# Kernel tuning notes

Hardware: AMD Instinct MI355X
Metric: run time of the kernel (lower is better)

The kernel has to match this reference:

```python
import jax, jax.numpy as jnp
import numpy as np

B, P, S, D, H, DFF, VOC = 16, 10, 128, 512, 8, 2048, 32000
SIGMA = 0.05
LN_EPS = 1e-6


def _ln(x, g, b):
    mu = jnp.mean(x, axis=-1, keepdims=True)
    var = jnp.var(x, axis=-1, keepdims=True)
    return g * (x - mu) / jnp.sqrt(var + LN_EPS) + b


def setup_inputs() -> dict:
    key = jax.random.key(0)
    ks = jax.random.split(key, 16)
    def wmat(k, shp):
        return (jax.random.normal(k, shp) * 0.02).astype(jnp.float32)
    return {
        "r": jax.random.normal(ks[0], (B, P, D), jnp.float32),
        "x": jax.random.randint(ks[1], (B,), 0, VOC),
        "K": jax.random.normal(ks[2], (B, P, S, D), jnp.float32),
        "V": jax.random.normal(ks[3], (B, P, S, D), jnp.float32),
        "w_state": jax.random.uniform(ks[4], (B, P, 1), jnp.float32),
        "I": jax.random.randint(ks[5], (B, P, S), 0, P),
        "t": 64,
        "Wq": wmat(ks[6], (D, D)), "bq": jnp.zeros((D,), jnp.float32),
        "Wk": wmat(ks[7], (D, D)), "bk": jnp.zeros((D,), jnp.float32),
        "Wv": wmat(ks[8], (D, D)), "bv": jnp.zeros((D,), jnp.float32),
        "Wo": wmat(ks[9], (D, D)), "bo": jnp.zeros((D,), jnp.float32),
        "W1": wmat(ks[10], (D, DFF)), "b1": jnp.zeros((DFF,), jnp.float32),
        "W2": wmat(ks[11], (DFF, D)), "b2": jnp.zeros((D,), jnp.float32),
        "g1": jnp.ones((D,), jnp.float32), "be1": jnp.zeros((D,), jnp.float32),
        "g3": jnp.ones((D,), jnp.float32), "be3": jnp.zeros((D,), jnp.float32),
        "Wout": wmat(ks[12], (D, VOC)), "bout": jnp.zeros((VOC,), jnp.float32),
    }


def reference(r, x, K, V, w_state, I, t, Wq, bq, Wk, bk, Wv, bv, Wo, bo,
              W1, b1, W2, b2, g1, be1, g3, be3, Wout, bout):
    k1, k2, k3, k4, k5 = jax.random.split(jax.random.key(42), 5)
    I = I.astype(jnp.int32)
    # particle resampling of attention state: gather along particle dim per timestep
    K = jnp.take_along_axis(K, I[..., None], axis=1)  # (B,P,S,D)
    V = jnp.take_along_axis(V, I[..., None], axis=1)
    rin = r[:, :, None, :]                            # (B,P,1,D)
    q = rin @ Wq + bq
    k = rin @ Wk + bk
    v = rin @ Wv + bv
    # SMC reparameterization noise on the projections
    q = q + SIGMA * jax.random.normal(k1, q.shape, q.dtype)
    k = k + SIGMA * jax.random.normal(k2, k.shape, k.dtype)
    v = v + SIGMA * jax.random.normal(k3, v.shape, v.dtype)
    # write current k, v into the attention state at position t
    K = jax.lax.dynamic_update_slice_in_dim(K, k, t, axis=2)
    V = jax.lax.dynamic_update_slice_in_dim(V, v, t, axis=2)
    dh = D // H
    qh = q.reshape(B, P, 1, H, dh).transpose(0, 1, 3, 2, 4)  # (B,P,H,1,dh)
    Kh = K.reshape(B, P, S, H, dh).transpose(0, 1, 3, 2, 4)  # (B,P,H,S,dh)
    Vh = V.reshape(B, P, S, H, dh).transpose(0, 1, 3, 2, 4)
    scores = jnp.einsum('bphqd,bphsd->bphqs', qh, Kh) / jnp.sqrt(jnp.asarray(dh, q.dtype))
    attn = jax.nn.softmax(scores, axis=-1)                   # (B,P,H,1,S)
    ctx = jnp.einsum('bphqs,bphsd->bphqd', attn, Vh)
    ctx = ctx.transpose(0, 1, 3, 2, 4).reshape(B, P, 1, D)
    z = ctx @ Wo + bo
    epsilon = SIGMA * jax.random.normal(k4, z.shape, z.dtype)  # stored stddev
    z = z + epsilon
    attn_weights = jnp.mean(attn, axis=2)                    # (B,P,1,S)
    out1 = _ln(z + rin, g1, be1)
    ffn = jax.nn.relu(out1 @ W1 + b1) @ W2 + b2
    out3 = _ln(ffn + out1, g3, be3)                          # (B,P,1,D)
    predictions = out3 @ Wout + bout                         # (B,P,1,VOC)
    # classification weight computation: softmax + gather at label x
    probs = jax.nn.softmax(predictions, axis=-1)
    w = jnp.take_along_axis(probs, x[:, None, None, None].astype(jnp.int32), axis=-1)[..., 0, 0]  # (B,P)
    w = jax.lax.stop_gradient(w)
    pred_sq = predictions[:, :, 0, :]                        # (B,P,VOC)
    average_prediction = jnp.sum(pred_sq * w[:, :, None], axis=1)[:, None, :]  # (B,1,VOC)
    argmax_w = jnp.argmax(w, axis=1)
    max_prediction = jnp.take_along_axis(pred_sq, argmax_w[:, None, None], axis=1)[:, 0, :]  # (B,VOC)
    # sample-and-keep-indices: categorical draw of P particle ancestors per batch
    i_t = jax.random.categorical(k5, w[:, None, :], axis=-1, shape=(B, P)).astype(jnp.int32)
    I_new = jax.lax.dynamic_update_slice_in_dim(I, i_t[:, :, None], t, axis=2)
    I_new = jax.lax.stop_gradient(I_new)
    # resample z with the freshly-sampled indices (I_new[:,:,t] == i_t)
    z = jnp.take_along_axis(z, i_t[:, :, None, None], axis=1)
    return out3, z, average_prediction, max_prediction, epsilon, attn_weights, K, V, w, I_new
```

## Files before the change

### kernel.cpp

```cpp
#include <hip/hip_runtime.h>
#include <cstdint>
#include <cstddef>

#define B_    16
#define P_    10
#define S_    128
#define D_    512
#define H_    8
#define DH_   64
#define DFF_  2048
#define VOC_  32000
#define NROW  160
#define SIGMA 0.05f
#define LN_EPS 1e-6f

struct U2 { uint32_t x, y; };

__host__ __device__ __forceinline__ U2 tf2x32(uint32_t k0, uint32_t k1,
                                              uint32_t x0, uint32_t x1) {
  uint32_t ks[3] = {k0, k1, k0 ^ k1 ^ 0x1BD11BDAu};
  x0 += ks[0]; x1 += ks[1];
  const int R0[4] = {13, 15, 26, 6};
  const int R1[4] = {17, 29, 16, 24};
#pragma unroll
  for (int i = 0; i < 5; ++i) {
    const int* r = (i & 1) ? R1 : R0;
#pragma unroll
    for (int j = 0; j < 4; ++j) {
      x0 += x1;
      x1 = (x1 << r[j]) | (x1 >> (32 - r[j]));
      x1 ^= x0;
    }
    x0 += ks[(i + 1) % 3];
    x1 += ks[(i + 2) % 3] + (uint32_t)(i + 1);
  }
  return {x0, x1};
}

__device__ __forceinline__ uint32_t jax_bits32(uint32_t k0, uint32_t k1, uint32_t j) {
  U2 o = tf2x32(k0, k1, 0u, j);
  return o.x ^ o.y;
}

__device__ __forceinline__ float erfinv32(float x) {
  float w = -log1pf(-x * x);
  float p;
  if (w < 5.0f) {
    w = w - 2.5f;
    p = 2.81022636e-08f;
    p = fmaf(p, w, 3.43273939e-07f);
    p = fmaf(p, w, -3.5233877e-06f);
    p = fmaf(p, w, -4.39150654e-06f);
    p = fmaf(p, w, 0.00021858087f);
    p = fmaf(p, w, -0.00125372503f);
    p = fmaf(p, w, -0.00417768164f);
    p = fmaf(p, w, 0.246640727f);
    p = fmaf(p, w, 1.50140941f);
  } else {
    w = sqrtf(w) - 3.0f;
    p = -0.000200214257f;
    p = fmaf(p, w, 0.000100950558f);
    p = fmaf(p, w, 0.00134934322f);
    p = fmaf(p, w, -0.00367342844f);
    p = fmaf(p, w, 0.00573950773f);
    p = fmaf(p, w, -0.0076224613f);
    p = fmaf(p, w, 0.00943887047f);
    p = fmaf(p, w, 1.00167406f);
    p = fmaf(p, w, 2.83297682f);
  }
  return p * x;
}

__device__ __forceinline__ float jax_normal(uint32_t k0, uint32_t k1, uint32_t j) {
  uint32_t b = jax_bits32(k0, k1, j);
  float u01 = __uint_as_float((b >> 9) | 0x3F800000u) - 1.0f;
  const float lo = -0.99999994f;
  float u = fmaxf(lo, fmaf(u01, 2.0f, lo));
  return 1.41421356f * erfinv32(u);
}

__device__ __forceinline__ float jax_gumbel(uint32_t k0, uint32_t k1, uint32_t j) {
  uint32_t b = jax_bits32(k0, k1, j);
  float u01 = __uint_as_float((b >> 9) | 0x3F800000u) - 1.0f;
  const float tiny = 1.17549435e-38f;
  float u = fmaxf(tiny, u01 + tiny);
  return -logf(-logf(u));
}


__global__ __launch_bounds__(256) void k_gather(const float* __restrict__ K,
                                                const float* __restrict__ V,
                                                const int* __restrict__ I,
                                                float* __restrict__ oK,
                                                float* __restrict__ oV) {
  size_t idx = (size_t)blockIdx.x * 256 + threadIdx.x;
  const size_t total = (size_t)NROW * S_ * (D_ / 4);
  if (idx >= total) return;
  int d4 = (int)(idx % (D_ / 4));
  size_t row = idx / (D_ / 4);
  int s = (int)(row % S_);
  int bp = (int)(row / S_);
  int b = bp / P_;
  int iv = I[row];
  size_t src = ((size_t)(b * P_ + iv) * S_ + s) * (D_ / 4) + d4;
  ((float4*)oK)[idx] = ((const float4*)K)[src];
  ((float4*)oV)[idx] = ((const float4*)V)[src];
}

__global__ __launch_bounds__(128) void k_qkvp(const float* __restrict__ r,
    const float* __restrict__ Wq, const float* __restrict__ bq,
    const float* __restrict__ Wk, const float* __restrict__ bk,
    const float* __restrict__ Wv, const float* __restrict__ bv,
    float* __restrict__ pq, float* __restrict__ pk, float* __restrict__ pv) {
  int c = blockIdx.x * 128 + threadIdx.x;
  int r0 = blockIdx.y * 4;
  int kc = blockIdx.z;
  int d0 = kc * 64;
  float aq[4], ak[4], av[4];
  float bbq = (kc == 0) ? bq[c] : 0.f;
  float bbk = (kc == 0) ? bk[c] : 0.f;
  float bbv = (kc == 0) ? bv[c] : 0.f;
#pragma unroll
  for (int rr = 0; rr < 4; ++rr) { aq[rr] = bbq; ak[rr] = bbk; av[rr] = bbv; }
  for (int d = d0; d < d0 + 64; d += 4) {
    float wq0 = Wq[(size_t)d * D_ + c],      wq1 = Wq[(size_t)(d+1) * D_ + c];
    float wq2 = Wq[(size_t)(d+2) * D_ + c],  wq3 = Wq[(size_t)(d+3) * D_ + c];
    float wk0 = Wk[(size_t)d * D_ + c],      wk1 = Wk[(size_t)(d+1) * D_ + c];
    float wk2 = Wk[(size_t)(d+2) * D_ + c],  wk3 = Wk[(size_t)(d+3) * D_ + c];
    float wv0 = Wv[(size_t)d * D_ + c],      wv1 = Wv[(size_t)(d+1) * D_ + c];
    float wv2 = Wv[(size_t)(d+2) * D_ + c],  wv3 = Wv[(size_t)(d+3) * D_ + c];
#pragma unroll
    for (int rr = 0; rr < 4; ++rr) {
      float4 a = *(const float4*)&r[(size_t)(r0 + rr) * D_ + d];
      aq[rr] = fmaf(a.w, wq3, fmaf(a.z, wq2, fmaf(a.y, wq1, fmaf(a.x, wq0, aq[rr]))));
      ak[rr] = fmaf(a.w, wk3, fmaf(a.z, wk2, fmaf(a.y, wk1, fmaf(a.x, wk0, ak[rr]))));
      av[rr] = fmaf(a.w, wv3, fmaf(a.z, wv2, fmaf(a.y, wv1, fmaf(a.x, wv0, av[rr]))));
    }
  }
#pragma unroll
  for (int rr = 0; rr < 4; ++rr) {
    size_t o = ((size_t)kc * NROW + r0 + rr) * D_ + c;
    pq[o] = aq[rr]; pk[o] = ak[rr]; pv[o] = av[rr];
  }
}

__global__ __launch_bounds__(256) void k_qkvr(const float* __restrict__ pq,
    const float* __restrict__ pk, const float* __restrict__ pv,
    const int* __restrict__ tptr, float* __restrict__ wsq,
    float* __restrict__ oK, float* __restrict__ oV,
    uint32_t k1a, uint32_t k1b, uint32_t k2a, uint32_t k2b,
    uint32_t k3a, uint32_t k3b) {
  int idx = blockIdx.x * 256 + threadIdx.x;
  if (idx >= NROW * D_) return;
  float q = pq[idx], k = pk[idx], v = pv[idx];
#pragma unroll
  for (int kc = 1; kc < 8; ++kc) {
    size_t o = (size_t)kc * (NROW * D_) + idx;
    q += pq[o]; k += pk[o]; v += pv[o];
  }
  int bp = idx / D_, c = idx % D_;
  int ts = min(max(*tptr, 0), S_ - 1);
  uint32_t j = (uint32_t)idx;
  wsq[idx] = q + SIGMA * jax_normal(k1a, k1b, j);
  oK[((size_t)bp * S_ + ts) * D_ + c] = k + SIGMA * jax_normal(k2a, k2b, j);
  oV[((size_t)bp * S_ + ts) * D_ + c] = v + SIGMA * jax_normal(k3a, k3b, j);
}

__global__ __launch_bounds__(128) void k_attn(const float* __restrict__ wsq,
    const float* __restrict__ oK, const float* __restrict__ oV,
    float* __restrict__ wsctx, float* __restrict__ wsattn) {
  __shared__ float s_q[DH_];
  __shared__ float s_attn[S_];
  __shared__ float red[S_];
  int bp = blockIdx.x >> 3, h = blockIdx.x & 7, tid = threadIdx.x;
  if (tid < DH_) s_q[tid] = wsq[bp * D_ + h * DH_ + tid];
  __syncthreads();
  const float4* krow = (const float4*)(oK + ((size_t)bp * S_ + tid) * D_ + h * DH_);
  const float4* q4 = (const float4*)s_q;
  float sc = 0.f;
#pragma unroll
  for (int d = 0; d < DH_ / 4; ++d) {
    float4 kv = krow[d], qv = q4[d];
    sc += qv.x * kv.x + qv.y * kv.y + qv.z * kv.z + qv.w * kv.w;
  }
  sc *= 0.125f;
  red[tid] = sc; __syncthreads();
  for (int s = 64; s > 0; s >>= 1) {
    if (tid < s) red[tid] = fmaxf(red[tid], red[tid + s]);
    __syncthreads();
  }
  float m = red[0]; __syncthreads();
  float e = expf(sc - m);
  red[tid] = e; __syncthreads();
  for (int s = 64; s > 0; s >>= 1) {
    if (tid < s) red[tid] += red[tid + s];
    __syncthreads();
  }
  float a = e / red[0];
  s_attn[tid] = a;
  wsattn[(size_t)blockIdx.x * S_ + tid] = a;
  __syncthreads();
  {
    int dd = tid & 63, sh = tid >> 6;
    const float* vb = oV + ((size_t)bp * S_ + sh * 64) * D_ + h * DH_ + dd;
    float acc = 0.f;
#pragma unroll 4
    for (int s = 0; s < 64; ++s) acc = fmaf(s_attn[sh * 64 + s], vb[(size_t)s * D_], acc);
    red[tid] = acc; __syncthreads();
    if (tid < DH_) wsctx[bp * D_ + h * DH_ + tid] = red[tid] + red[tid + 64];
  }
}

__global__ __launch_bounds__(256) void k_aw(const float* __restrict__ wsattn,
                                            float* __restrict__ oaw) {
  int idx = blockIdx.x * 256 + threadIdx.x;
  if (idx >= NROW * S_) return;
  int bp = idx / S_, s = idx % S_;
  float acc = 0.f;
#pragma unroll
  for (int h = 0; h < H_; ++h) acc += wsattn[(size_t)(bp * H_ + h) * S_ + s];
  oaw[idx] = acc * 0.125f;
}

__global__ __launch_bounds__(128) void k_zmatp(const float* __restrict__ wsctx,
    const float* __restrict__ Wo, const float* __restrict__ bo,
    float* __restrict__ pz) {
  int c = blockIdx.x * 128 + threadIdx.x;
  int r0 = blockIdx.y * 4;
  int kc = blockIdx.z;
  int d0 = kc * 64;
  float acc[4];
  float bb = (kc == 0) ? bo[c] : 0.f;
#pragma unroll
  for (int rr = 0; rr < 4; ++rr) acc[rr] = bb;
  for (int d = d0; d < d0 + 64; d += 4) {
    float w0 = Wo[(size_t)d * D_ + c],     w1 = Wo[(size_t)(d+1) * D_ + c];
    float w2 = Wo[(size_t)(d+2) * D_ + c], w3 = Wo[(size_t)(d+3) * D_ + c];
#pragma unroll
    for (int rr = 0; rr < 4; ++rr) {
      float4 a = *(const float4*)&wsctx[(size_t)(r0 + rr) * D_ + d];
      acc[rr] = fmaf(a.w, w3, fmaf(a.z, w2, fmaf(a.y, w1, fmaf(a.x, w0, acc[rr]))));
    }
  }
#pragma unroll
  for (int rr = 0; rr < 4; ++rr)
    pz[((size_t)kc * NROW + r0 + rr) * D_ + c] = acc[rr];
}

__global__ __launch_bounds__(256) void k_zmatr(const float* __restrict__ pz,
    const float* __restrict__ r, float* __restrict__ oeps,
    float* __restrict__ wsz, float* __restrict__ wsx,
    uint32_t k4a, uint32_t k4b) {
  int idx = blockIdx.x * 256 + threadIdx.x;
  if (idx >= NROW * D_) return;
  float s = pz[idx];
#pragma unroll
  for (int kc = 1; kc < 8; ++kc) s += pz[(size_t)kc * (NROW * D_) + idx];
  uint32_t j = (uint32_t)idx;
  float eps = SIGMA * jax_normal(k4a, k4b, j);
  oeps[idx] = eps;
  float z = s + eps;
  wsz[idx] = z;
  wsx[idx] = z + r[idx];
}

__global__ __launch_bounds__(256) void k_ln(const float* __restrict__ wsx,
    const float* __restrict__ g, const float* __restrict__ b,
    float* __restrict__ o) {
  __shared__ float red[256];
  int bp = blockIdx.x, tid = threadIdx.x;
  float x0 = wsx[bp * D_ + tid], x1 = wsx[bp * D_ + tid + 256];
  red[tid] = x0 + x1; __syncthreads();
  for (int s = 128; s > 0; s >>= 1) { if (tid < s) red[tid] += red[tid + s]; __syncthreads(); }
  float mu = red[0] / (float)D_; __syncthreads();
  float d0 = x0 - mu, d1 = x1 - mu;
  red[tid] = d0 * d0 + d1 * d1; __syncthreads();
  for (int s = 128; s > 0; s >>= 1) { if (tid < s) red[tid] += red[tid + s]; __syncthreads(); }
  float inv = 1.0f / sqrtf(red[0] / (float)D_ + LN_EPS);
  o[bp * D_ + tid] = g[tid] * d0 * inv + b[tid];
  o[bp * D_ + tid + 256] = g[tid + 256] * d1 * inv + b[tid + 256];
}

__global__ __launch_bounds__(128) void k_ffn1p(const float* __restrict__ wsout1,
    const float* __restrict__ W1, const float* __restrict__ b1,
    float* __restrict__ pf) {
  int c = blockIdx.x * 128 + threadIdx.x;
  int r0 = blockIdx.y * 8;
  int kc = blockIdx.z;
  int d0 = kc * 128;
  float acc[8];
  float bb = (kc == 0) ? b1[c] : 0.f;
#pragma unroll
  for (int rr = 0; rr < 8; ++rr) acc[rr] = bb;
  for (int d = d0; d < d0 + 128; d += 4) {
    float w0 = W1[(size_t)d * DFF_ + c],     w1 = W1[(size_t)(d+1) * DFF_ + c];
    float w2 = W1[(size_t)(d+2) * DFF_ + c], w3 = W1[(size_t)(d+3) * DFF_ + c];
#pragma unroll
    for (int rr = 0; rr < 8; ++rr) {
      float4 a = *(const float4*)&wsout1[(size_t)(r0 + rr) * D_ + d];
      acc[rr] = fmaf(a.w, w3, fmaf(a.z, w2, fmaf(a.y, w1, fmaf(a.x, w0, acc[rr]))));
    }
  }
#pragma unroll
  for (int rr = 0; rr < 8; ++rr)
    pf[((size_t)kc * NROW + r0 + rr) * DFF_ + c] = acc[rr];
}

__global__ __launch_bounds__(256) void k_ffn1r(const float* __restrict__ pf,
    float* __restrict__ wsffn) {
  int idx = blockIdx.x * 256 + threadIdx.x;
  if (idx >= NROW * DFF_) return;
  float s = pf[idx];
#pragma unroll
  for (int kc = 1; kc < 4; ++kc) s += pf[(size_t)kc * (NROW * DFF_) + idx];
  wsffn[idx] = fmaxf(s, 0.f);
}

__global__ __launch_bounds__(128) void k_ffn2p(const float* __restrict__ wsffn,
    const float* __restrict__ W2, float* __restrict__ p2) {
  int c = blockIdx.x * 128 + threadIdx.x;
  int r0 = blockIdx.y * 4;
  int kc = blockIdx.z;
  int d0 = kc * 128;
  float acc[4];
#pragma unroll
  for (int rr = 0; rr < 4; ++rr) acc[rr] = 0.f;
  for (int d = d0; d < d0 + 128; d += 4) {
    float w0 = W2[(size_t)d * D_ + c],     w1 = W2[(size_t)(d+1) * D_ + c];
    float w2 = W2[(size_t)(d+2) * D_ + c], w3 = W2[(size_t)(d+3) * D_ + c];
#pragma unroll
    for (int rr = 0; rr < 4; ++rr) {
      float4 a = *(const float4*)&wsffn[(size_t)(r0 + rr) * DFF_ + d];
      acc[rr] = fmaf(a.w, w3, fmaf(a.z, w2, fmaf(a.y, w1, fmaf(a.x, w0, acc[rr]))));
    }
  }
#pragma unroll
  for (int rr = 0; rr < 4; ++rr)
    p2[((size_t)kc * NROW + r0 + rr) * D_ + c] = acc[rr];
}

__global__ __launch_bounds__(256) void k_ffn2r(const float* __restrict__ p2,
    const float* __restrict__ b2, const float* __restrict__ wsout1,
    float* __restrict__ wsx) {
  int idx = blockIdx.x * 256 + threadIdx.x;
  if (idx >= NROW * D_) return;
  float s = p2[idx];
#pragma unroll
  for (int kc = 1; kc < 16; ++kc) s += p2[(size_t)kc * (NROW * D_) + idx];
  int c = idx % D_;
  wsx[idx] = s + b2[c] + wsout1[idx];
}

__global__ __launch_bounds__(256, 4) void k_preds(const float* __restrict__ A,
    const float* __restrict__ Wout, const float* __restrict__ bout,
    float* __restrict__ wspred) {
  __shared__ float sA[80][68];
  int tid = threadIdx.x;
  int cb = blockIdx.x, rh = blockIdx.y;
  int cg = tid & 15, rg = tid >> 4;
  int c = cb * 64 + cg * 4;
  float4 acc[5];
  {
    float4 b0 = *(const float4*)&bout[c];
#pragma unroll
    for (int i = 0; i < 5; ++i) acc[i] = b0;
  }
  const float* Ab = A + (size_t)rh * 80 * D_;
  for (int d0 = 0; d0 < D_; d0 += 64) {
    if (d0) __syncthreads();
#pragma unroll
    for (int k = 0; k < 5; ++k) {
      int idx = tid + k * 256;
      int row = idx >> 4, c4 = idx & 15;
      *(float4*)&sA[row][c4 * 4] =
          *(const float4*)&Ab[(size_t)row * D_ + d0 + c4 * 4];
    }
    __syncthreads();
#pragma unroll 2
    for (int dd = 0; dd < 64; dd += 4) {
      size_t wb = (size_t)(d0 + dd) * VOC_ + c;
      float4 w0 = *(const float4*)&Wout[wb];
      float4 w1 = *(const float4*)&Wout[wb + VOC_];
      float4 w2 = *(const float4*)&Wout[wb + 2 * (size_t)VOC_];
      float4 w3 = *(const float4*)&Wout[wb + 3 * (size_t)VOC_];
#pragma unroll
      for (int i = 0; i < 5; ++i) {
        float4 a = *(const float4*)&sA[rg * 5 + i][dd];
        acc[i].x = fmaf(a.x, w0.x, acc[i].x); acc[i].y = fmaf(a.x, w0.y, acc[i].y);
        acc[i].z = fmaf(a.x, w0.z, acc[i].z); acc[i].w = fmaf(a.x, w0.w, acc[i].w);
        acc[i].x = fmaf(a.y, w1.x, acc[i].x); acc[i].y = fmaf(a.y, w1.y, acc[i].y);
        acc[i].z = fmaf(a.y, w1.z, acc[i].z); acc[i].w = fmaf(a.y, w1.w, acc[i].w);
        acc[i].x = fmaf(a.z, w2.x, acc[i].x); acc[i].y = fmaf(a.z, w2.y, acc[i].y);
        acc[i].z = fmaf(a.z, w2.z, acc[i].z); acc[i].w = fmaf(a.z, w2.w, acc[i].w);
        acc[i].x = fmaf(a.w, w3.x, acc[i].x); acc[i].y = fmaf(a.w, w3.y, acc[i].y);
        acc[i].z = fmaf(a.w, w3.z, acc[i].z); acc[i].w = fmaf(a.w, w3.w, acc[i].w);
      }
    }
  }
#pragma unroll
  for (int i = 0; i < 5; ++i) {
    size_t o = (size_t)(rh * 80 + rg * 5 + i) * VOC_ + c;
    *(float4*)&wspred[o] = acc[i];
  }
}

__global__ __launch_bounds__(256) void k_stats(const float* __restrict__ wspred,
    const int* __restrict__ x, float* __restrict__ ow) {
  __shared__ float red[256];
  int bp = blockIdx.x, tid = threadIdx.x;
  const float* row = wspred + (size_t)bp * VOC_;
  const float4* row4 = (const float4*)row;
  float m = -INFINITY;
  for (int i = tid; i < VOC_ / 4; i += 256) {
    float4 v = row4[i];
    m = fmaxf(m, fmaxf(fmaxf(v.x, v.y), fmaxf(v.z, v.w)));
  }
  red[tid] = m; __syncthreads();
  for (int s = 128; s > 0; s >>= 1) { if (tid < s) red[tid] = fmaxf(red[tid], red[tid + s]); __syncthreads(); }
  m = red[0]; __syncthreads();
  float sum = 0.f;
  for (int i = tid; i < VOC_ / 4; i += 256) {
    float4 v = row4[i];
    sum += expf(v.x - m) + expf(v.y - m) + expf(v.z - m) + expf(v.w - m);
  }
  red[tid] = sum; __syncthreads();
  for (int s = 128; s > 0; s >>= 1) { if (tid < s) red[tid] += red[tid + s]; __syncthreads(); }
  if (tid == 0) {
    int b = bp / P_;
    ow[bp] = expf(row[x[b]] - m) / red[0];
  }
}

__global__ __launch_bounds__(256) void k_it(const float* __restrict__ ow,
    int* __restrict__ wsit, int* __restrict__ wsamw,
    uint32_t k5a, uint32_t k5b) {
  int tid = threadIdx.x;
  if (tid < NROW) {
    int b = tid / P_;
    float best = -INFINITY; int bi = 0;
#pragma unroll
    for (int i = 0; i < P_; ++i) {
      float g = jax_gumbel(k5a, k5b, (uint32_t)(tid * P_ + i));
      float v = g + ow[b * P_ + i];
      if (v > best) { best = v; bi = i; }
    }
    wsit[tid] = bi;
  }
  if (tid < B_) {
    float best = -INFINITY; int bi = 0;
#pragma unroll
    for (int p = 0; p < P_; ++p) {
      float v = ow[tid * P_ + p];
      if (v > best) { best = v; bi = p; }
    }
    wsamw[tid] = bi;
  }
}

__global__ __launch_bounds__(256) void k_avgmax(const float* __restrict__ wspred,
    const float* __restrict__ ow, const int* __restrict__ wsamw,
    float* __restrict__ oavg, float* __restrict__ omax) {
  int idx = blockIdx.x * 256 + threadIdx.x;
  if (idx >= B_ * VOC_) return;
  int b = idx / VOC_, c = idx % VOC_;
  float acc = 0.f;
#pragma unroll
  for (int p = 0; p < P_; ++p)
    acc = fmaf(wspred[(size_t)(b * P_ + p) * VOC_ + c], ow[b * P_ + p], acc);
  oavg[idx] = acc;
  omax[idx] = wspred[(size_t)(b * P_ + wsamw[b]) * VOC_ + c];
}

__global__ __launch_bounds__(256) void k_zsel(const float* __restrict__ wsz,
    const int* __restrict__ wsit, const int* __restrict__ I,
    const int* __restrict__ tptr, float* __restrict__ oz, float* __restrict__ oI) {
  int idx = blockIdx.x * 256 + threadIdx.x;
  if (idx < NROW * D_) {
    int bp = idx / D_, d = idx % D_;
    int b = bp / P_;
    oz[idx] = wsz[(size_t)(b * P_ + wsit[bp]) * D_ + d];
  }
  if (idx < NROW * S_) {
    int bp = idx / S_, s = idx % S_;
    int ts = min(max(*tptr, 0), S_ - 1);
    oI[idx] = (s == ts) ? (float)wsit[bp] : (float)I[idx];
  }
}

static void derive_keys(uint32_t keys[5][2]) {
  for (int i = 0; i < 5; ++i) {
    U2 o = tf2x32(0u, 42u, 0u, (uint32_t)i);
    keys[i][0] = o.x; keys[i][1] = o.y;
  }
}

extern "C" void kernel_launch(void* const* d_in, const int* in_sizes, int n_in,
                              void* d_out, int out_size, void* d_ws, size_t ws_size,
                              hipStream_t stream) {
  const float* r   = (const float*)d_in[0];
  const int*   x   = (const int*)d_in[1];
  const float* K   = (const float*)d_in[2];
  const float* V   = (const float*)d_in[3];
  const int*   I   = (const int*)d_in[5];
  const int*   tp  = (const int*)d_in[6];
  const float* Wq  = (const float*)d_in[7];
  const float* bq  = (const float*)d_in[8];
  const float* Wk  = (const float*)d_in[9];
  const float* bk  = (const float*)d_in[10];
  const float* Wv  = (const float*)d_in[11];
  const float* bv  = (const float*)d_in[12];
  const float* Wo  = (const float*)d_in[13];
  const float* bo  = (const float*)d_in[14];
  const float* W1  = (const float*)d_in[15];
  const float* b1  = (const float*)d_in[16];
  const float* W2  = (const float*)d_in[17];
  const float* b2  = (const float*)d_in[18];
  const float* g1  = (const float*)d_in[19];
  const float* be1 = (const float*)d_in[20];
  const float* g3  = (const float*)d_in[21];
  const float* be3 = (const float*)d_in[22];
  const float* Wout = (const float*)d_in[23];
  const float* bout = (const float*)d_in[24];

  float* out = (float*)d_out;
  const size_t O_OUT3 = 0;
  const size_t O_Z    = 81920;
  const size_t O_AVG  = 163840;
  const size_t O_MAX  = 675840;
  const size_t O_EPS  = 1187840;
  const size_t O_AW   = 1269760;
  const size_t O_K    = 1290240;
  const size_t O_V    = 11776000;
  const size_t O_W    = 22261760;
  const size_t O_I    = 22261920;

  float* ws = (float*)d_ws;
  const size_t W_Q    = 0;
  const size_t W_CTX  = 81920;
  const size_t W_Z    = 163840;
  const size_t W_OUT1 = 245760;
  const size_t W_ATT  = 327680;
  const size_t W_FFN  = 491520;
  const size_t W_PRED = 819200;
  const size_t W_IT   = 5939200;
  const size_t W_AMW  = 5939360;
  const size_t W_X    = W_Q;

  uint32_t kk[5][2];
  derive_keys(kk);

  float* oK = out + O_K;
  float* oV = out + O_V;
  float* sc = ws + W_PRED;

  k_gather<<<10240, 256, 0, stream>>>(K, V, I, oK, oV);
  k_qkvp<<<dim3(4, 40, 8), 128, 0, stream>>>(r, Wq, bq, Wk, bk, Wv, bv,
                                             sc, sc + 655360, sc + 1310720);
  k_qkvr<<<320, 256, 0, stream>>>(sc, sc + 655360, sc + 1310720, tp,
                                  ws + W_Q, oK, oV,
                                  kk[0][0], kk[0][1], kk[1][0], kk[1][1],
                                  kk[2][0], kk[2][1]);
  k_attn<<<NROW * H_, 128, 0, stream>>>(ws + W_Q, oK, oV, ws + W_CTX, ws + W_ATT);
  k_aw<<<(NROW * S_ + 255) / 256, 256, 0, stream>>>(ws + W_ATT, out + O_AW);
  k_zmatp<<<dim3(4, 40, 8), 128, 0, stream>>>(ws + W_CTX, Wo, bo, sc);
  k_zmatr<<<320, 256, 0, stream>>>(sc, r, out + O_EPS, ws + W_Z, ws + W_X,
                                   kk[3][0], kk[3][1]);
  k_ln<<<NROW, 256, 0, stream>>>(ws + W_X, g1, be1, ws + W_OUT1);
  k_ffn1p<<<dim3(16, 20, 4), 128, 0, stream>>>(ws + W_OUT1, W1, b1, sc);
  k_ffn1r<<<1280, 256, 0, stream>>>(sc, ws + W_FFN);
  k_ffn2p<<<dim3(4, 40, 16), 128, 0, stream>>>(ws + W_FFN, W2, sc);
  k_ffn2r<<<320, 256, 0, stream>>>(sc, b2, ws + W_OUT1, ws + W_X);
  k_ln<<<NROW, 256, 0, stream>>>(ws + W_X, g3, be3, out + O_OUT3);
  k_preds<<<dim3(500, 2), 256, 0, stream>>>(out + O_OUT3, Wout, bout, ws + W_PRED);
  k_stats<<<NROW, 256, 0, stream>>>(ws + W_PRED, x, out + O_W);
  k_it<<<1, 256, 0, stream>>>(out + O_W, (int*)(ws + W_IT), (int*)(ws + W_AMW),
                              kk[4][0], kk[4][1]);
  k_avgmax<<<(B_ * VOC_ + 255) / 256, 256, 0, stream>>>(ws + W_PRED, out + O_W,
                                                        (const int*)(ws + W_AMW),
                                                        out + O_AVG, out + O_MAX);
  k_zsel<<<(NROW * D_ + 255) / 256, 256, 0, stream>>>(ws + W_Z, (const int*)(ws + W_IT),
                                                      I, tp, out + O_Z, out + O_I);
}
```

Measured before the change: 444.5 us.

## Fuse reductions into layernorm, prefetch Wout in preds, merge tail kernels

Folds the split-K reductions for the z-projection and FFN2 directly into the layernorm kernels, and merges the avg/max and z-select/I-update kernels into one launch. Together these remove three kernel launches and the intermediate round-trips through workspace. The vocab projection now double-buffers Wout rows in registers and lowers its occupancy hint from 4 to 3 blocks to make room. The extra register pressure in k_preds could reduce latency hiding, and the fused layernorm kernels run with fewer blocks (160 instead of 320) for the reduction part.

```diff
diff --git a/kernel.cpp b/kernel.cpp
--- a/kernel.cpp
+++ b/kernel.cpp
@@ -247,29 +247,36 @@
     pz[((size_t)kc * NROW + r0 + rr) * D_ + c] = acc[rr];
 }
 
-__global__ __launch_bounds__(256) void k_zmatr(const float* __restrict__ pz,
-    const float* __restrict__ r, float* __restrict__ oeps,
-    float* __restrict__ wsz, float* __restrict__ wsx,
+__global__ __launch_bounds__(256) void k_zmatr_ln(const float* __restrict__ pz,
+    const float* __restrict__ r, const float* __restrict__ g,
+    const float* __restrict__ b, float* __restrict__ oeps,
+    float* __restrict__ wsz, float* __restrict__ o,
     uint32_t k4a, uint32_t k4b) {
-  int idx = blockIdx.x * 256 + threadIdx.x;
-  if (idx >= NROW * D_) return;
-  float s = pz[idx];
-#pragma unroll
-  for (int kc = 1; kc < 8; ++kc) s += pz[(size_t)kc * (NROW * D_) + idx];
-  uint32_t j = (uint32_t)idx;
-  float eps = SIGMA * jax_normal(k4a, k4b, j);
-  oeps[idx] = eps;
-  float z = s + eps;
-  wsz[idx] = z;
-  wsx[idx] = z + r[idx];
-}
-
-__global__ __launch_bounds__(256) void k_ln(const float* __restrict__ wsx,
-    const float* __restrict__ g, const float* __restrict__ b,
-    float* __restrict__ o) {
   __shared__ float red[256];
   int bp = blockIdx.x, tid = threadIdx.x;
-  float x0 = wsx[bp * D_ + tid], x1 = wsx[bp * D_ + tid + 256];
+  float x0, x1;
+  {
+    int idx = bp * D_ + tid;
+    float s = pz[idx];
+#pragma unroll
+    for (int kc = 1; kc < 8; ++kc) s += pz[(size_t)kc * (NROW * D_) + idx];
+    float eps = SIGMA * jax_normal(k4a, k4b, (uint32_t)idx);
+    oeps[idx] = eps;
+    float z = s + eps;
+    wsz[idx] = z;
+    x0 = z + r[idx];
+  }
+  {
+    int idx = bp * D_ + tid + 256;
+    float s = pz[idx];
+#pragma unroll
+    for (int kc = 1; kc < 8; ++kc) s += pz[(size_t)kc * (NROW * D_) + idx];
+    float eps = SIGMA * jax_normal(k4a, k4b, (uint32_t)idx);
+    oeps[idx] = eps;
+    float z = s + eps;
+    wsz[idx] = z;
+    x1 = z + r[idx];
+  }
   red[tid] = x0 + x1; __syncthreads();
   for (int s = 128; s > 0; s >>= 1) { if (tid < s) red[tid] += red[tid + s]; __syncthreads(); }
   float mu = red[0] / (float)D_; __syncthreads();
@@ -339,19 +346,39 @@
     p2[((size_t)kc * NROW + r0 + rr) * D_ + c] = acc[rr];
 }
 
-__global__ __launch_bounds__(256) void k_ffn2r(const float* __restrict__ p2,
+__global__ __launch_bounds__(256) void k_ffn2r_ln(const float* __restrict__ p2,
     const float* __restrict__ b2, const float* __restrict__ wsout1,
-    float* __restrict__ wsx) {
-  int idx = blockIdx.x * 256 + threadIdx.x;
-  if (idx >= NROW * D_) return;
-  float s = p2[idx];
-#pragma unroll
-  for (int kc = 1; kc < 16; ++kc) s += p2[(size_t)kc * (NROW * D_) + idx];
-  int c = idx % D_;
-  wsx[idx] = s + b2[c] + wsout1[idx];
-}
-
-__global__ __launch_bounds__(256, 4) void k_preds(const float* __restrict__ A,
+    const float* __restrict__ g, const float* __restrict__ b,
+    float* __restrict__ o) {
+  __shared__ float red[256];
+  int bp = blockIdx.x, tid = threadIdx.x;
+  float x0, x1;
+  {
+    int idx = bp * D_ + tid;
+    float s = p2[idx];
+#pragma unroll
+    for (int kc = 1; kc < 16; ++kc) s += p2[(size_t)kc * (NROW * D_) + idx];
+    x0 = s + b2[tid] + wsout1[idx];
+  }
+  {
+    int idx = bp * D_ + tid + 256;
+    float s = p2[idx];
+#pragma unroll
+    for (int kc = 1; kc < 16; ++kc) s += p2[(size_t)kc * (NROW * D_) + idx];
+    x1 = s + b2[tid + 256] + wsout1[idx];
+  }
+  red[tid] = x0 + x1; __syncthreads();
+  for (int s = 128; s > 0; s >>= 1) { if (tid < s) red[tid] += red[tid + s]; __syncthreads(); }
+  float mu = red[0] / (float)D_; __syncthreads();
+  float d0 = x0 - mu, d1 = x1 - mu;
+  red[tid] = d0 * d0 + d1 * d1; __syncthreads();
+  for (int s = 128; s > 0; s >>= 1) { if (tid < s) red[tid] += red[tid + s]; __syncthreads(); }
+  float inv = 1.0f / sqrtf(red[0] / (float)D_ + LN_EPS);
+  o[bp * D_ + tid] = g[tid] * d0 * inv + b[tid];
+  o[bp * D_ + tid + 256] = g[tid + 256] * d1 * inv + b[tid + 256];
+}
+
+__global__ __launch_bounds__(256, 3) void k_preds(const float* __restrict__ A,
     const float* __restrict__ Wout, const float* __restrict__ bout,
     float* __restrict__ wspred) {
   __shared__ float sA[80][68];
@@ -359,42 +386,64 @@
   int cb = blockIdx.x, rh = blockIdx.y;
   int cg = tid & 15, rg = tid >> 4;
   int c = cb * 64 + cg * 4;
+  int srow = tid >> 4, sc4 = tid & 15;
+  const float* Ab = A + (size_t)rh * 80 * D_;
+  const float* Wp = Wout + c;
   float4 acc[5];
   {
     float4 b0 = *(const float4*)&bout[c];
 #pragma unroll
     for (int i = 0; i < 5; ++i) acc[i] = b0;
   }
-  const float* Ab = A + (size_t)rh * 80 * D_;
-  for (int d0 = 0; d0 < D_; d0 += 64) {
-    if (d0) __syncthreads();
-#pragma unroll
-    for (int k = 0; k < 5; ++k) {
-      int idx = tid + k * 256;
-      int row = idx >> 4, c4 = idx & 15;
-      *(float4*)&sA[row][c4 * 4] =
-          *(const float4*)&Ab[(size_t)row * D_ + d0 + c4 * 4];
-    }
+  float4 c0[4], c1[4], n0[4], n1[4];
+#pragma unroll
+  for (int q = 0; q < 4; ++q) c0[q] = *(const float4*)&Wp[(size_t)q * VOC_];
+#pragma unroll
+  for (int q = 0; q < 4; ++q) c1[q] = *(const float4*)&Wp[(size_t)(4 + q) * VOC_];
+  for (int t = 0; t < 8; ++t) {
+    int d0 = t * 64;
+    if (t) __syncthreads();
+#pragma unroll
+    for (int k = 0; k < 5; ++k)
+      *(float4*)&sA[srow + k * 16][sc4 * 4] =
+          *(const float4*)&Ab[(size_t)(srow + k * 16) * D_ + d0 + sc4 * 4];
     __syncthreads();
-#pragma unroll 2
-    for (int dd = 0; dd < 64; dd += 4) {
-      size_t wb = (size_t)(d0 + dd) * VOC_ + c;
-      float4 w0 = *(const float4*)&Wout[wb];
-      float4 w1 = *(const float4*)&Wout[wb + VOC_];
-      float4 w2 = *(const float4*)&Wout[wb + 2 * (size_t)VOC_];
-      float4 w3 = *(const float4*)&Wout[wb + 3 * (size_t)VOC_];
+#pragma unroll
+    for (int u = 0; u < 8; ++u) {
+      int d = d0 + u * 8;
+      int dd = u * 8;
+#pragma unroll
+      for (int q = 0; q < 4; ++q)
+        n0[q] = *(const float4*)&Wp[(size_t)min(d + 8 + q, D_ - 1) * VOC_];
+#pragma unroll
+      for (int q = 0; q < 4; ++q)
+        n1[q] = *(const float4*)&Wp[(size_t)min(d + 12 + q, D_ - 1) * VOC_];
 #pragma unroll
       for (int i = 0; i < 5; ++i) {
         float4 a = *(const float4*)&sA[rg * 5 + i][dd];
-        acc[i].x = fmaf(a.x, w0.x, acc[i].x); acc[i].y = fmaf(a.x, w0.y, acc[i].y);
-        acc[i].z = fmaf(a.x, w0.z, acc[i].z); acc[i].w = fmaf(a.x, w0.w, acc[i].w);
-        acc[i].x = fmaf(a.y, w1.x, acc[i].x); acc[i].y = fmaf(a.y, w1.y, acc[i].y);
-        acc[i].z = fmaf(a.y, w1.z, acc[i].z); acc[i].w = fmaf(a.y, w1.w, acc[i].w);
-        acc[i].x = fmaf(a.z, w2.x, acc[i].x); acc[i].y = fmaf(a.z, w2.y, acc[i].y);
-        acc[i].z = fmaf(a.z, w2.z, acc[i].z); acc[i].w = fmaf(a.z, w2.w, acc[i].w);
-        acc[i].x = fmaf(a.w, w3.x, acc[i].x); acc[i].y = fmaf(a.w, w3.y, acc[i].y);
-        acc[i].z = fmaf(a.w, w3.z, acc[i].z); acc[i].w = fmaf(a.w, w3.w, acc[i].w);
+        acc[i].x = fmaf(a.x, c0[0].x, acc[i].x); acc[i].y = fmaf(a.x, c0[0].y, acc[i].y);
+        acc[i].z = fmaf(a.x, c0[0].z, acc[i].z); acc[i].w = fmaf(a.x, c0[0].w, acc[i].w);
+        acc[i].x = fmaf(a.y, c0[1].x, acc[i].x); acc[i].y = fmaf(a.y, c0[1].y, acc[i].y);
+        acc[i].z = fmaf(a.y, c0[1].z, acc[i].z); acc[i].w = fmaf(a.y, c0[1].w, acc[i].w);
+        acc[i].x = fmaf(a.z, c0[2].x, acc[i].x); acc[i].y = fmaf(a.z, c0[2].y, acc[i].y);
+        acc[i].z = fmaf(a.z, c0[2].z, acc[i].z); acc[i].w = fmaf(a.z, c0[2].w, acc[i].w);
+        acc[i].x = fmaf(a.w, c0[3].x, acc[i].x); acc[i].y = fmaf(a.w, c0[3].y, acc[i].y);
+        acc[i].z = fmaf(a.w, c0[3].z, acc[i].z); acc[i].w = fmaf(a.w, c0[3].w, acc[i].w);
       }
+#pragma unroll
+      for (int i = 0; i < 5; ++i) {
+        float4 a = *(const float4*)&sA[rg * 5 + i][dd + 4];
+        acc[i].x = fmaf(a.x, c1[0].x, acc[i].x); acc[i].y = fmaf(a.x, c1[0].y, acc[i].y);
+        acc[i].z = fmaf(a.x, c1[0].z, acc[i].z); acc[i].w = fmaf(a.x, c1[0].w, acc[i].w);
+        acc[i].x = fmaf(a.y, c1[1].x, acc[i].x); acc[i].y = fmaf(a.y, c1[1].y, acc[i].y);
+        acc[i].z = fmaf(a.y, c1[1].z, acc[i].z); acc[i].w = fmaf(a.y, c1[1].w, acc[i].w);
+        acc[i].x = fmaf(a.z, c1[2].x, acc[i].x); acc[i].y = fmaf(a.z, c1[2].y, acc[i].y);
+        acc[i].z = fmaf(a.z, c1[2].z, acc[i].z); acc[i].w = fmaf(a.z, c1[2].w, acc[i].w);
+        acc[i].x = fmaf(a.w, c1[3].x, acc[i].x); acc[i].y = fmaf(a.w, c1[3].y, acc[i].y);
+        acc[i].z = fmaf(a.w, c1[3].z, acc[i].z); acc[i].w = fmaf(a.w, c1[3].w, acc[i].w);
+      }
+#pragma unroll
+      for (int q = 0; q < 4; ++q) { c0[q] = n0[q]; c1[q] = n1[q]; }
     }
   }
 #pragma unroll
@@ -457,33 +506,35 @@
   }
 }
 
-__global__ __launch_bounds__(256) void k_avgmax(const float* __restrict__ wspred,
+__global__ __launch_bounds__(256) void k_tail(const float* __restrict__ wspred,
     const float* __restrict__ ow, const int* __restrict__ wsamw,
-    float* __restrict__ oavg, float* __restrict__ omax) {
-  int idx = blockIdx.x * 256 + threadIdx.x;
-  if (idx >= B_ * VOC_) return;
-  int b = idx / VOC_, c = idx % VOC_;
-  float acc = 0.f;
-#pragma unroll
-  for (int p = 0; p < P_; ++p)
-    acc = fmaf(wspred[(size_t)(b * P_ + p) * VOC_ + c], ow[b * P_ + p], acc);
-  oavg[idx] = acc;
-  omax[idx] = wspred[(size_t)(b * P_ + wsamw[b]) * VOC_ + c];
-}
-
-__global__ __launch_bounds__(256) void k_zsel(const float* __restrict__ wsz,
-    const int* __restrict__ wsit, const int* __restrict__ I,
-    const int* __restrict__ tptr, float* __restrict__ oz, float* __restrict__ oI) {
-  int idx = blockIdx.x * 256 + threadIdx.x;
-  if (idx < NROW * D_) {
-    int bp = idx / D_, d = idx % D_;
-    int b = bp / P_;
-    oz[idx] = wsz[(size_t)(b * P_ + wsit[bp]) * D_ + d];
-  }
-  if (idx < NROW * S_) {
-    int bp = idx / S_, s = idx % S_;
-    int ts = min(max(*tptr, 0), S_ - 1);
-    oI[idx] = (s == ts) ? (float)wsit[bp] : (float)I[idx];
+    const float* __restrict__ wsz, const int* __restrict__ wsit,
+    const int* __restrict__ I, const int* __restrict__ tptr,
+    float* __restrict__ oavg, float* __restrict__ omax,
+    float* __restrict__ oz, float* __restrict__ oI) {
+  int bid = blockIdx.x, tid = threadIdx.x;
+  if (bid < 2000) {
+    int idx = bid * 256 + tid;
+    if (idx >= B_ * VOC_) return;
+    int b = idx / VOC_, c = idx % VOC_;
+    float acc = 0.f;
+#pragma unroll
+    for (int p = 0; p < P_; ++p)
+      acc = fmaf(wspred[(size_t)(b * P_ + p) * VOC_ + c], ow[b * P_ + p], acc);
+    oavg[idx] = acc;
+    omax[idx] = wspred[(size_t)(b * P_ + wsamw[b]) * VOC_ + c];
+  } else {
+    int idx = (bid - 2000) * 256 + tid;
+    if (idx < NROW * D_) {
+      int bp = idx / D_, d = idx % D_;
+      int b = bp / P_;
+      oz[idx] = wsz[(size_t)(b * P_ + wsit[bp]) * D_ + d];
+    }
+    if (idx < NROW * S_) {
+      int bp = idx / S_, s = idx % S_;
+      int ts = min(max(*tptr, 0), S_ - 1);
+      oI[idx] = (s == ts) ? (float)wsit[bp] : (float)I[idx];
+    }
   }
 }
 
@@ -544,7 +595,6 @@
   const size_t W_PRED = 819200;
   const size_t W_IT   = 5939200;
   const size_t W_AMW  = 5939360;
-  const size_t W_X    = W_Q;
 
   uint32_t kk[5][2];
   derive_keys(kk);
@@ -563,21 +613,19 @@
   k_attn<<<NROW * H_, 128, 0, stream>>>(ws + W_Q, oK, oV, ws + W_CTX, ws + W_ATT);
   k_aw<<<(NROW * S_ + 255) / 256, 256, 0, stream>>>(ws + W_ATT, out + O_AW);
   k_zmatp<<<dim3(4, 40, 8), 128, 0, stream>>>(ws + W_CTX, Wo, bo, sc);
-  k_zmatr<<<320, 256, 0, stream>>>(sc, r, out + O_EPS, ws + W_Z, ws + W_X,
-                                   kk[3][0], kk[3][1]);
-  k_ln<<<NROW, 256, 0, stream>>>(ws + W_X, g1, be1, ws + W_OUT1);
+  k_zmatr_ln<<<NROW, 256, 0, stream>>>(sc, r, g1, be1, out + O_EPS, ws + W_Z,
+                                       ws + W_OUT1, kk[3][0], kk[3][1]);
   k_ffn1p<<<dim3(16, 20, 4), 128, 0, stream>>>(ws + W_OUT1, W1, b1, sc);
   k_ffn1r<<<1280, 256, 0, stream>>>(sc, ws + W_FFN);
   k_ffn2p<<<dim3(4, 40, 16), 128, 0, stream>>>(ws + W_FFN, W2, sc);
-  k_ffn2r<<<320, 256, 0, stream>>>(sc, b2, ws + W_OUT1, ws + W_X);
-  k_ln<<<NROW, 256, 0, stream>>>(ws + W_X, g3, be3, out + O_OUT3);
+  k_ffn2r_ln<<<NROW, 256, 0, stream>>>(sc, b2, ws + W_OUT1, g3, be3, out + O_OUT3);
   k_preds<<<dim3(500, 2), 256, 0, stream>>>(out + O_OUT3, Wout, bout, ws + W_PRED);
   k_stats<<<NROW, 256, 0, stream>>>(ws + W_PRED, x, out + O_W);
   k_it<<<1, 256, 0, stream>>>(out + O_W, (int*)(ws + W_IT), (int*)(ws + W_AMW),
                               kk[4][0], kk[4][1]);
-  k_avgmax<<<(B_ * VOC_ + 255) / 256, 256, 0, stream>>>(ws + W_PRED, out + O_W,
-                                                        (const int*)(ws + W_AMW),
-                                                        out + O_AVG, out + O_MAX);
-  k_zsel<<<(NROW * D_ + 255) / 256, 256, 0, stream>>>(ws + W_Z, (const int*)(ws + W_IT),
-                                                      I, tp, out + O_Z, out + O_I);
-}
+  k_tail<<<2320, 256, 0, stream>>>(ws + W_PRED, out + O_W,
+                                   (const int*)(ws + W_AMW), ws + W_Z,
+                                   (const int*)(ws + W_IT), I, tp,
+                                   out + O_AVG, out + O_MAX,
+                                   out + O_Z, out + O_I);
+}
```

Measured after the change: 549.2 us. 1.24x slower.
